# Kernel tuning notes

Hardware: AMD Instinct MI355X
Metric: run time of the kernel (lower is better)

The kernel has to match this reference:

```python
import jax, jax.numpy as jnp
import numpy as np

N_NODES = 100000
N_EDGES = 1600000
N_GRAPHS = 512
NEG_SLOPE = 0.2  # PyG GATConv default


def setup_inputs() -> dict:
    key = jax.random.key(0)
    ks = jax.random.split(key, 12)
    x = jax.random.normal(ks[0], (N_NODES, 75), dtype=jnp.float32)
    edge_index = jax.random.randint(ks[1], (2, N_EDGES), 0, N_NODES, dtype=jnp.int64 if jax.config.jax_enable_x64 else jnp.int32)
    batch = jnp.sort(jax.random.randint(ks[2], (N_NODES,), 0, N_GRAPHS, dtype=jnp.int32))
    s = lambda k, shp, fan: jax.random.normal(k, shp, dtype=jnp.float32) * (1.0 / np.sqrt(fan))
    return {
        "x": x, "edge_index": edge_index, "batch": batch,
        "W1": s(ks[3], (75, 64), 75),           # conv1: heads=8, out=8
        "att_src1": s(ks[4], (8, 8), 8),
        "att_dst1": s(ks[5], (8, 8), 8),
        "bias1": jnp.zeros((64,), jnp.float32),
        "W2": s(ks[6], (64, 128), 64),          # conv2: heads=1, out=128
        "att_src2": s(ks[7], (1, 128), 128),
        "att_dst2": s(ks[8], (1, 128), 128),
        "bias2": jnp.zeros((128,), jnp.float32),
        "Wg": s(ks[9], (128, 1), 128),
        "bg": jnp.zeros((1,), jnp.float32),
    }


def _gat_conv(x, src, dst, W, att_src, att_dst, bias, heads, out_ch):
    # x: [N, F_in]; edges src->dst (self-loops already included)
    n = x.shape[0]
    h = (x @ W).reshape(n, heads, out_ch)            # [N, H, C]
    a_src = (h * att_src).sum(-1)                    # [N, H]
    a_dst = (h * att_dst).sum(-1)                    # [N, H]
    e = a_src[src] + a_dst[dst]                      # [E, H]
    e = jax.nn.leaky_relu(e, NEG_SLOPE)
    # segment softmax over incoming edges of each dst node
    emax = jax.ops.segment_max(e, dst, num_segments=n)      # [N, H]
    ee = jnp.exp(e - emax[dst])
    denom = jax.ops.segment_sum(ee, dst, num_segments=n)    # [N, H]
    alpha = ee / denom[dst]                                  # [E, H]
    msg = h[src] * alpha[:, :, None]                          # [E, H, C]
    out = jax.ops.segment_sum(msg, dst, num_segments=n)      # [N, H, C]
    return out.reshape(n, heads * out_ch) + bias


def reference(x, edge_index, batch, W1, att_src1, att_dst1, bias1,
              W2, att_src2, att_dst2, bias2, Wg, bg):
    n = x.shape[0]
    # PyG GATConv adds self-loops by default
    loops = jnp.arange(n, dtype=edge_index.dtype)
    src = jnp.concatenate([edge_index[0], loops])
    dst = jnp.concatenate([edge_index[1], loops])
    # eval mode: dropout is identity
    x2 = jax.nn.elu(_gat_conv(x, src, dst, W1, att_src1, att_dst1, bias1, heads=8, out_ch=8))
    x4 = _gat_conv(x2, src, dst, W2, att_src2, att_dst2, bias2, heads=1, out_ch=128)
    y = jax.ops.segment_sum(x4, batch, num_segments=N_GRAPHS)  # global_add_pool
    return y @ Wg + bg  # [N_GRAPHS, 1]
```

## Files before the change

### kernel.cpp

```cpp
#include <hip/hip_runtime.h>
#include <hip/hip_bf16.h>
#include <math.h>

#define N_NODES 100000
#define N_EDGES 1600000
#define ET (N_EDGES + N_NODES)
#define N_GRAPHS 512
#define NEG_SLOPE 0.2f
#define G1_BLOCKS 2048
#define G2_BLOCKS 1280
#define F1_BLOCKS 2048

#define BSH 8
#define NBUCK ((N_NODES + 255) / 256)
#define BCAP 5120
#define ABLK 1024
#define CHUNK ((ET + ABLK - 1) / ABLK)

__device__ __forceinline__ void atomAddF(float* p, float v) { unsafeAtomicAdd(p, v); }
__device__ __forceinline__ float lrelu(float v) { return v >= 0.f ? v : NEG_SLOPE * v; }

__device__ __forceinline__ unsigned short f2bf(float f) {
    unsigned int u = __float_as_uint(f);
    u += 0x7FFFu + ((u >> 16) & 1u);
    return (unsigned short)(u >> 16);
}
__device__ __forceinline__ float bf2f(unsigned short s) { return __uint_as_float(((unsigned int)s) << 16); }
__device__ __forceinline__ float bflo(unsigned int p) { return __uint_as_float(p << 16); }
__device__ __forceinline__ float bfhi(unsigned int p) { return __uint_as_float(p & 0xFFFF0000u); }

__global__ __launch_bounds__(256) void k_pre(
    const int* __restrict__ ei, uint2* __restrict__ gbuf, int* __restrict__ bcur,
    const float* __restrict__ W2, const float* __restrict__ as2,
    const float* __restrict__ ad2, const float* __restrict__ Wg,
    const float* __restrict__ b2, const float* __restrict__ bg,
    float* __restrict__ wv, float* __restrict__ out)
{
    __shared__ __align__(16) char smem[CHUNK * 8 + NBUCK * 16];
    const int t = threadIdx.x;

    if (blockIdx.x >= ABLK) {
        const int bb = blockIdx.x - ABLK;
        if (bb > 0) {
            int i = (bb - 1) * 256 + t;
            if (i < N_GRAPHS) out[i] = bg[0];
            return;
        }
        if (t < 192) {
            int c = t & 63, which = t >> 6;
            const float* v = (which == 0) ? Wg : ((which == 1) ? as2 : ad2);
            float s = 0.f;
            #pragma unroll
            for (int k = 0; k < 128; ++k) s += W2[c * 128 + k] * v[k];
            wv[which * 64 + c] = s;
        } else if (t == 192) {
            float s = 0.f;
            #pragma unroll
            for (int k = 0; k < 128; ++k) s += b2[k] * Wg[k];
            wv[192] = s;
        }
        return;
    }

    uint2* pairs = (uint2*)smem;
    int* hist  = (int*)(smem + CHUNK * 8);
    int* excl  = hist + NBUCK;
    int* gbase = excl + NBUCK;
    int* cnt2  = gbase + NBUCK;
    const long e0 = (long)blockIdx.x * CHUNK;
    const int  n  = (int)((e0 + CHUNK <= ET) ? CHUNK : (ET - e0));
    for (int i = t; i < NBUCK; i += 256) { hist[i] = 0; cnt2[i] = 0; }
    __syncthreads();
    for (int i = t; i < n; i += 256) {
        long e = e0 + i;
        int dst = (e < N_EDGES) ? ei[N_EDGES + e] : (int)(e - N_EDGES);
        atomicAdd(&hist[dst >> BSH], 1);
    }
    __syncthreads();
    if (t == 0) {
        int acc = 0;
        for (int b = 0; b < NBUCK; ++b) { excl[b] = acc; acc += hist[b]; }
    }
    __syncthreads();
    for (int i = t; i < n; i += 256) {
        long e = e0 + i;
        int src, dst;
        if (e < N_EDGES) { src = ei[e]; dst = ei[N_EDGES + e]; }
        else             { src = dst = (int)(e - N_EDGES); }
        int b = dst >> BSH;
        int pos = excl[b] + atomicAdd(&cnt2[b], 1);
        pairs[pos] = make_uint2((unsigned)src, (unsigned)dst);
    }
    __syncthreads();
    for (int b = t; b < NBUCK; b += 256)
        gbase[b] = hist[b] ? atomicAdd(&bcur[b], hist[b]) : 0;
    __syncthreads();
    for (int i = t; i < n; i += 256) {
        uint2 pr = pairs[i];
        int b = (int)(pr.y >> BSH);
        gbuf[(long)b * BCAP + gbase[b] + (i - excl[b])] = pr;
    }
}

__global__ __launch_bounds__(256) void k_mid(
    const uint2* __restrict__ gbuf, const int* __restrict__ bcur,
    int* __restrict__ rowptr, int* __restrict__ ecol,
    const float* __restrict__ x, const float* __restrict__ W1,
    const float* __restrict__ as1, const float* __restrict__ ad1,
    unsigned short* __restrict__ h1p, unsigned short* __restrict__ a1sh,
    float* __restrict__ a1d)
{
    __shared__ __align__(16) char smem[4096];
    const int t = threadIdx.x;

    if (blockIdx.x >= NBUCK) {
        float (*xs)[76] = (float (*)[76])smem;
        const int g = t >> 6;
        const int c = t & 63;
        const int vb = blockIdx.x - NBUCK;
        for (int nb = vb; nb < N_NODES / 4; nb += F1_BLOCKS) {
            const int n = nb * 4 + g;
            const float* xr = x + (long)n * 75;
            xs[g][c] = xr[c];
            if (c < 11) xs[g][64 + c] = xr[64 + c];
            __syncthreads();
            float h = 0.f;
            #pragma unroll
            for (int k = 0; k < 75; ++k) h += xs[g][k] * W1[k * 64 + c];
            h1p[(long)n * 64 + c] = f2bf(h);
            const int head = c >> 3, lane = c & 7;
            float vs = h * as1[c];
            float vd = h * ad1[c];
            #pragma unroll
            for (int off = 1; off < 8; off <<= 1) {
                vs += __shfl_xor(vs, off, 64);
                vd += __shfl_xor(vd, off, 64);
            }
            if (lane == 0) { a1sh[n * 8 + head] = f2bf(vs); a1d[n * 8 + head] = vd; }
            __syncthreads();
        }
        return;
    }

    int* hist = (int*)smem;
    int* excl = hist + 256;
    int* cnt2 = excl + 256;
    int* red  = cnt2 + 256;
    const int b = blockIdx.x;
    const int cnt  = bcur[b];
    const int d0 = b << BSH;
    const int nloc = (N_NODES - d0 < 256) ? (N_NODES - d0) : 256;

    int partial = 0;
    for (int i = t; i < b; i += 256) partial += bcur[i];
    red[t] = partial;
    __syncthreads();
    for (int off = 128; off > 0; off >>= 1) {
        if (t < off) red[t] += red[t + off];
        __syncthreads();
    }
    const int base = red[0];

    if (t < nloc) { hist[t] = 0; cnt2[t] = 0; }
    __syncthreads();
    const uint2* eb = gbuf + (long)b * BCAP;
    for (int i = t; i < cnt; i += 256) atomicAdd(&hist[(int)eb[i].y - d0], 1);
    __syncthreads();
    if (t == 0) {
        int acc = 0;
        for (int k = 0; k < nloc; ++k) { excl[k] = acc; acc += hist[k]; }
    }
    __syncthreads();
    if (t < nloc) rowptr[d0 + t] = base + excl[t];
    if (b == NBUCK - 1 && t == 0) rowptr[N_NODES] = base + cnt;
    for (int i = t; i < cnt; i += 256) {
        uint2 pr = eb[i];
        int dl = (int)pr.y - d0;
        int slot = excl[dl] + atomicAdd(&cnt2[dl], 1);
        ecol[base + slot] = (int)pr.x;
    }
}

__global__ __launch_bounds__(256) void k_gat1(
    const int* __restrict__ rowptr, const int* __restrict__ ecol,
    const unsigned short* __restrict__ a1sh, const float* __restrict__ a1d,
    const unsigned short* __restrict__ h1p, const float* __restrict__ bias1,
    const float* __restrict__ wv,
    float2* __restrict__ sg2, float* __restrict__ a2dv)
{
    const int slot = threadIdx.x >> 6;
    const int lane = threadIdx.x & 63;
    const int g = lane >> 3;
    const int l = lane & 7;
    const int stride = gridDim.x * 4;

    for (int base = blockIdx.x * 4; base < N_NODES; base += stride) {
        const int dst = base + slot;
        const int beg = rowptr[dst], end = rowptr[dst + 1];
        const float adh = a1d[(long)dst * 8 + l];

        float acc[8] = {0.f,0.f,0.f,0.f,0.f,0.f,0.f,0.f};
        float den = 0.f;

        int j = beg + g;
        bool v = (j < end);
        int s = v ? ecol[j] : 0;
        unsigned short ab = a1sh[(long)s * 8 + l];
        uint4 pv = *(const uint4*)(h1p + (long)s * 64 + l * 8);

        for (int j0 = beg; j0 < end; j0 += 8) {
            int jn = j + 8;
            bool vn = (jn < end);
            int sn = vn ? ecol[jn] : 0;
            unsigned short abn = a1sh[(long)sn * 8 + l];
            uint4 pvn = *(const uint4*)(h1p + (long)sn * 64 + l * 8);
            float ee = v ? __expf(lrelu(bf2f(ab) + adh)) : 0.f;
            den += ee;
            acc[0] += ee * bflo(pv.x); acc[1] += ee * bfhi(pv.x);
            acc[2] += ee * bflo(pv.y); acc[3] += ee * bfhi(pv.y);
            acc[4] += ee * bflo(pv.z); acc[5] += ee * bfhi(pv.z);
            acc[6] += ee * bflo(pv.w); acc[7] += ee * bfhi(pv.w);
            j = jn; v = vn; s = sn; ab = abn; pv = pvn;
        }
        #pragma unroll
        for (int off = 8; off <= 32; off <<= 1) {
            den += __shfl_xor(den, off, 64);
            #pragma unroll
            for (int k = 0; k < 8; ++k) acc[k] += __shfl_xor(acc[k], off, 64);
        }

        if (g == 0) {
            const float inv = 1.f / den;
            float pg = 0.f, ps = 0.f, pd = 0.f;
            #pragma unroll
            for (int k = 0; k < 8; ++k) {
                float vv = acc[k] * inv + bias1[l * 8 + k];
                vv = vv > 0.f ? vv : (__expf(vv) - 1.f);
                pg += vv * wv[l * 8 + k];
                ps += vv * wv[64 + l * 8 + k];
                pd += vv * wv[128 + l * 8 + k];
            }
            #pragma unroll
            for (int off = 1; off < 8; off <<= 1) {
                pg += __shfl_xor(pg, off, 64);
                ps += __shfl_xor(ps, off, 64);
                pd += __shfl_xor(pd, off, 64);
            }
            if (l == 0) { sg2[dst] = make_float2(ps, pg); a2dv[dst] = pd; }
        }
    }
}

__global__ __launch_bounds__(256) void k_gat2(
    const int* __restrict__ rowptr, const int* __restrict__ ecol,
    const float2* __restrict__ sg2, const float* __restrict__ a2dv,
    const float* __restrict__ wv, const int* __restrict__ batch,
    float* __restrict__ out)
{
    const int lane = threadIdx.x & 63;
    const int sl = lane & 15;
    const int sgid = ((blockIdx.x * 256 + threadIdx.x) >> 4);
    const int NS = G2_BLOCKS * 16;
    const int per = (N_NODES + NS - 1) / NS;
    const int n0 = sgid * per;
    const int n1 = min(n0 + per, N_NODES);
    const float bc = wv[192];

    float accg = 0.f;
    int curg = -1;
    for (int n = n0; n < n1; ++n) {
        const int beg = rowptr[n], end = rowptr[n + 1];
        const float adv = a2dv[n];
        float num = 0.f, den = 0.f;
        for (int j = beg + sl; j < end; j += 16) {
            int s = ecol[j];
            float2 v = sg2[s];
            float ee = __expf(lrelu(v.x + adv));
            den += ee;
            num += ee * v.y;
        }
        #pragma unroll
        for (int off = 1; off < 16; off <<= 1) {
            den += __shfl_xor(den, off, 64);
            num += __shfl_xor(num, off, 64);
        }
        if (sl == 0) {
            int gr = batch[n];
            if (gr != curg) {
                if (curg >= 0) atomAddF(out + curg, accg);
                curg = gr; accg = 0.f;
            }
            accg += num / den + bc;
        }
    }
    if (sl == 0 && curg >= 0) atomAddF(out + curg, accg);
}

extern "C" void kernel_launch(void* const* d_in, const int* in_sizes, int n_in,
                              void* d_out, int out_size, void* d_ws, size_t ws_size,
                              hipStream_t stream) {
    (void)in_sizes; (void)n_in; (void)out_size; (void)ws_size;
    const float* x     = (const float*)d_in[0];
    const int*   ei    = (const int*)d_in[1];
    const int*   batch = (const int*)d_in[2];
    const float* W1    = (const float*)d_in[3];
    const float* as1   = (const float*)d_in[4];
    const float* ad1   = (const float*)d_in[5];
    const float* b1    = (const float*)d_in[6];
    const float* W2    = (const float*)d_in[7];
    const float* as2   = (const float*)d_in[8];
    const float* ad2   = (const float*)d_in[9];
    const float* b2    = (const float*)d_in[10];
    const float* Wg    = (const float*)d_in[11];
    const float* bg    = (const float*)d_in[12];
    float* out = (float*)d_out;

    const long N = N_NODES;
    char* p = (char*)d_ws;
    int* rowptr = (int*)p;              p += (N + 4)        * sizeof(int);
    int* bcur   = (int*)p;              p += 512            * sizeof(int);
    int* ecol   = (int*)p;              p += (long)ET       * sizeof(int);
    uint2* gbuf = (uint2*)p;            p += (long)NBUCK * BCAP * sizeof(uint2);
    unsigned short* h1p  = (unsigned short*)p; p += N * 64  * sizeof(unsigned short);
    unsigned short* a1sh = (unsigned short*)p; p += N * 8   * sizeof(unsigned short);
    float* a1d  = (float*)p;            p += N * 8          * sizeof(float);
    float2* sg2 = (float2*)p;           p += N              * sizeof(float2);
    float* a2dv = (float*)p;            p += N              * sizeof(float);
    float* wv   = (float*)p;            p += 256            * sizeof(float);

    hipMemsetAsync(bcur, 0, NBUCK * sizeof(int), stream);
    k_pre <<<ABLK + 3, 256, 0, stream>>>(ei, gbuf, bcur,
                                         W2, as2, ad2, Wg, b2, bg, wv, out);
    k_mid <<<NBUCK + F1_BLOCKS, 256, 0, stream>>>(gbuf, bcur, rowptr, ecol,
                                                  x, W1, as1, ad1, h1p, a1sh, a1d);
    k_gat1<<<G1_BLOCKS, 256, 0, stream>>>(rowptr, ecol, a1sh, a1d, h1p, b1, wv, sg2, a2dv);
    k_gat2<<<G2_BLOCKS, 256, 0, stream>>>(rowptr, ecol, sg2, a2dv, wv, batch, out);
}
```

Before: 311.8 us.

## Fuse CSR bucket finalize into gat1 and move x@W1 into pre kernel

Moves the first-layer feature transform into the edge-bucketing kernel, so it runs alongside the histogram work. It also fuses the per-bucket CSR build into the first GAT kernel, keeping each bucket's column list in LDS for the aggregation. Buckets shrink to 128 destinations and the single-thread serial prefix scans become parallel scans. This removes one launch and the global ecol re-read in gat1, but leaves only one block per 128 nodes, with 512 threads and larger LDS use, which may limit occupancy and load balance.

After: 281.2 us. 1.11x faster.

```diff
diff --git a/kernel.cpp b/kernel.cpp
--- a/kernel.cpp
+++ b/kernel.cpp
@@ -7,15 +7,16 @@
 #define ET (N_EDGES + N_NODES)
 #define N_GRAPHS 512
 #define NEG_SLOPE 0.2f
-#define G1_BLOCKS 2048
 #define G2_BLOCKS 1280
-#define F1_BLOCKS 2048
-
-#define BSH 8
-#define NBUCK ((N_NODES + 255) / 256)
-#define BCAP 5120
-#define ABLK 1024
+
+#define BSH 7
+#define NDB 128
+#define NBUCK ((N_NODES + NDB - 1) / NDB)
+#define BCAP 2560
+#define ABLK 512
 #define CHUNK ((ET + ABLK - 1) / ABLK)
+#define F1_OFF (ABLK + 3)
+#define PRE_GRID (F1_OFF + 1536)
 
 __device__ __forceinline__ void atomAddF(float* p, float v) { unsafeAtomicAdd(p, v); }
 __device__ __forceinline__ float lrelu(float v) { return v >= 0.f ? v : NEG_SLOPE * v; }
@@ -31,33 +32,67 @@
 
 __global__ __launch_bounds__(256) void k_pre(
     const int* __restrict__ ei, uint2* __restrict__ gbuf, int* __restrict__ bcur,
+    const float* __restrict__ x, const float* __restrict__ W1,
+    const float* __restrict__ as1, const float* __restrict__ ad1,
     const float* __restrict__ W2, const float* __restrict__ as2,
     const float* __restrict__ ad2, const float* __restrict__ Wg,
     const float* __restrict__ b2, const float* __restrict__ bg,
-    float* __restrict__ wv, float* __restrict__ out)
+    unsigned short* __restrict__ h1p, unsigned short* __restrict__ a1sh,
+    float* __restrict__ a1d, float* __restrict__ wv, float* __restrict__ out)
 {
-    __shared__ __align__(16) char smem[CHUNK * 8 + NBUCK * 16];
+    __shared__ __align__(16) char smem[CHUNK * 8 + NBUCK * 16 + 1024];
     const int t = threadIdx.x;
-
-    if (blockIdx.x >= ABLK) {
-        const int bb = blockIdx.x - ABLK;
-        if (bb > 0) {
+    const int blk = blockIdx.x;
+
+    if (blk >= ABLK && blk < F1_OFF) {
+        const int bb = blk - ABLK;
+        if (bb == 0) {
+            if (t < 192) {
+                int c = t & 63, which = t >> 6;
+                const float* v = (which == 0) ? Wg : ((which == 1) ? as2 : ad2);
+                float s = 0.f;
+                #pragma unroll
+                for (int k = 0; k < 128; ++k) s += W2[c * 128 + k] * v[k];
+                wv[which * 64 + c] = s;
+            } else if (t == 192) {
+                float s = 0.f;
+                #pragma unroll
+                for (int k = 0; k < 128; ++k) s += b2[k] * Wg[k];
+                wv[192] = s;
+            }
+        } else {
             int i = (bb - 1) * 256 + t;
             if (i < N_GRAPHS) out[i] = bg[0];
-            return;
-        }
-        if (t < 192) {
-            int c = t & 63, which = t >> 6;
-            const float* v = (which == 0) ? Wg : ((which == 1) ? as2 : ad2);
-            float s = 0.f;
-            #pragma unroll
-            for (int k = 0; k < 128; ++k) s += W2[c * 128 + k] * v[k];
-            wv[which * 64 + c] = s;
-        } else if (t == 192) {
-            float s = 0.f;
-            #pragma unroll
-            for (int k = 0; k < 128; ++k) s += b2[k] * Wg[k];
-            wv[192] = s;
+        }
+        return;
+    }
+
+    if (blk >= F1_OFF) {
+        float (*xs)[76] = (float (*)[76])smem;
+        const int g = t >> 6;
+        const int c = t & 63;
+        const int vb = blk - F1_OFF;
+        const int fstride = PRE_GRID - F1_OFF;
+        for (int nb = vb; nb < N_NODES / 4; nb += fstride) {
+            const int n = nb * 4 + g;
+            const float* xr = x + (long)n * 75;
+            xs[g][c] = xr[c];
+            if (c < 11) xs[g][64 + c] = xr[64 + c];
+            __syncthreads();
+            float h = 0.f;
+            #pragma unroll
+            for (int k = 0; k < 75; ++k) h += xs[g][k] * W1[k * 64 + c];
+            h1p[(long)n * 64 + c] = f2bf(h);
+            const int head = c >> 3, lane = c & 7;
+            float vs = h * as1[c];
+            float vd = h * ad1[c];
+            #pragma unroll
+            for (int off = 1; off < 8; off <<= 1) {
+                vs += __shfl_xor(vs, off, 64);
+                vd += __shfl_xor(vd, off, 64);
+            }
+            if (lane == 0) { a1sh[n * 8 + head] = f2bf(vs); a1d[n * 8 + head] = vd; }
+            __syncthreads();
         }
         return;
     }
@@ -67,7 +102,8 @@
     int* excl  = hist + NBUCK;
     int* gbase = excl + NBUCK;
     int* cnt2  = gbase + NBUCK;
-    const long e0 = (long)blockIdx.x * CHUNK;
+    int* red   = cnt2 + NBUCK;
+    const long e0 = (long)blk * CHUNK;
     const int  n  = (int)((e0 + CHUNK <= ET) ? CHUNK : (ET - e0));
     for (int i = t; i < NBUCK; i += 256) { hist[i] = 0; cnt2[i] = 0; }
     __syncthreads();
@@ -77,9 +113,28 @@
         atomicAdd(&hist[dst >> BSH], 1);
     }
     __syncthreads();
-    if (t == 0) {
-        int acc = 0;
-        for (int b = 0; b < NBUCK; ++b) { excl[b] = acc; acc += hist[b]; }
+    {
+        int lk[4]; int s = 0;
+        #pragma unroll
+        for (int k = 0; k < 4; ++k) {
+            int idx = t * 4 + k;
+            int v = (idx < NBUCK) ? hist[idx] : 0;
+            lk[k] = s; s += v;
+        }
+        red[t] = s;
+        __syncthreads();
+        for (int off = 1; off < 256; off <<= 1) {
+            int a = (t >= off) ? red[t - off] : 0;
+            __syncthreads();
+            red[t] += a;
+            __syncthreads();
+        }
+        int p = red[t] - s;
+        #pragma unroll
+        for (int k = 0; k < 4; ++k) {
+            int idx = t * 4 + k;
+            if (idx < NBUCK) excl[idx] = p + lk[k];
+        }
     }
     __syncthreads();
     for (int i = t; i < n; i += 256) {
@@ -102,101 +157,71 @@
     }
 }
 
-__global__ __launch_bounds__(256) void k_mid(
+__global__ __launch_bounds__(512) void k_gat1(
     const uint2* __restrict__ gbuf, const int* __restrict__ bcur,
     int* __restrict__ rowptr, int* __restrict__ ecol,
-    const float* __restrict__ x, const float* __restrict__ W1,
-    const float* __restrict__ as1, const float* __restrict__ ad1,
-    unsigned short* __restrict__ h1p, unsigned short* __restrict__ a1sh,
-    float* __restrict__ a1d)
-{
-    __shared__ __align__(16) char smem[4096];
-    const int t = threadIdx.x;
-
-    if (blockIdx.x >= NBUCK) {
-        float (*xs)[76] = (float (*)[76])smem;
-        const int g = t >> 6;
-        const int c = t & 63;
-        const int vb = blockIdx.x - NBUCK;
-        for (int nb = vb; nb < N_NODES / 4; nb += F1_BLOCKS) {
-            const int n = nb * 4 + g;
-            const float* xr = x + (long)n * 75;
-            xs[g][c] = xr[c];
-            if (c < 11) xs[g][64 + c] = xr[64 + c];
-            __syncthreads();
-            float h = 0.f;
-            #pragma unroll
-            for (int k = 0; k < 75; ++k) h += xs[g][k] * W1[k * 64 + c];
-            h1p[(long)n * 64 + c] = f2bf(h);
-            const int head = c >> 3, lane = c & 7;
-            float vs = h * as1[c];
-            float vd = h * ad1[c];
-            #pragma unroll
-            for (int off = 1; off < 8; off <<= 1) {
-                vs += __shfl_xor(vs, off, 64);
-                vd += __shfl_xor(vd, off, 64);
-            }
-            if (lane == 0) { a1sh[n * 8 + head] = f2bf(vs); a1d[n * 8 + head] = vd; }
-            __syncthreads();
-        }
-        return;
-    }
-
-    int* hist = (int*)smem;
-    int* excl = hist + 256;
-    int* cnt2 = excl + 256;
-    int* red  = cnt2 + 256;
-    const int b = blockIdx.x;
-    const int cnt  = bcur[b];
-    const int d0 = b << BSH;
-    const int nloc = (N_NODES - d0 < 256) ? (N_NODES - d0) : 256;
-
-    int partial = 0;
-    for (int i = t; i < b; i += 256) partial += bcur[i];
-    red[t] = partial;
-    __syncthreads();
-    for (int off = 128; off > 0; off >>= 1) {
-        if (t < off) red[t] += red[t + off];
-        __syncthreads();
-    }
-    const int base = red[0];
-
-    if (t < nloc) { hist[t] = 0; cnt2[t] = 0; }
-    __syncthreads();
-    const uint2* eb = gbuf + (long)b * BCAP;
-    for (int i = t; i < cnt; i += 256) atomicAdd(&hist[(int)eb[i].y - d0], 1);
-    __syncthreads();
-    if (t == 0) {
-        int acc = 0;
-        for (int k = 0; k < nloc; ++k) { excl[k] = acc; acc += hist[k]; }
-    }
-    __syncthreads();
-    if (t < nloc) rowptr[d0 + t] = base + excl[t];
-    if (b == NBUCK - 1 && t == 0) rowptr[N_NODES] = base + cnt;
-    for (int i = t; i < cnt; i += 256) {
-        uint2 pr = eb[i];
-        int dl = (int)pr.y - d0;
-        int slot = excl[dl] + atomicAdd(&cnt2[dl], 1);
-        ecol[base + slot] = (int)pr.x;
-    }
-}
-
-__global__ __launch_bounds__(256) void k_gat1(
-    const int* __restrict__ rowptr, const int* __restrict__ ecol,
     const unsigned short* __restrict__ a1sh, const float* __restrict__ a1d,
     const unsigned short* __restrict__ h1p, const float* __restrict__ bias1,
     const float* __restrict__ wv,
     float2* __restrict__ sg2, float* __restrict__ a2dv)
 {
-    const int slot = threadIdx.x >> 6;
-    const int lane = threadIdx.x & 63;
+    __shared__ int lds_ecol[BCAP];
+    __shared__ int hist[NDB], excl[NDB + 1], cnt2[NDB];
+    __shared__ int red[512];
+    const int t = threadIdx.x;
+    const int b = blockIdx.x;
+    const int d0 = b << BSH;
+    const int nloc = (N_NODES - d0 < NDB) ? (N_NODES - d0) : NDB;
+    const int cnt = bcur[b];
+
+    int partial = 0;
+    for (int i = t; i < b; i += 512) partial += bcur[i];
+    red[t] = partial;
+    __syncthreads();
+    for (int off = 256; off > 0; off >>= 1) {
+        if (t < off) red[t] += red[t + off];
+        __syncthreads();
+    }
+    const int base = red[0];
+    __syncthreads();
+
+    if (t < NDB) { hist[t] = 0; cnt2[t] = 0; }
+    __syncthreads();
+    const uint2* eb = gbuf + (long)b * BCAP;
+    for (int i = t; i < cnt; i += 512) atomicAdd(&hist[(int)eb[i].y - d0], 1);
+    __syncthreads();
+    {
+        int v = (t < NDB) ? hist[t] : 0;
+        if (t < NDB) red[t] = v;
+        __syncthreads();
+        for (int off = 1; off < NDB; off <<= 1) {
+            int a = (t < NDB && t >= off) ? red[t - off] : 0;
+            __syncthreads();
+            if (t < NDB) red[t] += a;
+            __syncthreads();
+        }
+        if (t < nloc) excl[t] = red[t] - v;
+        if (t == 0) excl[nloc] = cnt;
+    }
+    __syncthreads();
+    if (t < nloc) rowptr[d0 + t] = base + excl[t];
+    if (b == NBUCK - 1 && t == 0) rowptr[N_NODES] = base + cnt;
+    for (int i = t; i < cnt; i += 512) {
+        uint2 pr = eb[i];
+        int dl = (int)pr.y - d0;
+        int slot = excl[dl] + atomicAdd(&cnt2[dl], 1);
+        lds_ecol[slot] = (int)pr.x;
+    }
+    __syncthreads();
+    for (int i = t; i < cnt; i += 512) ecol[base + i] = lds_ecol[i];
+
+    const int wave = t >> 6;
+    const int lane = t & 63;
     const int g = lane >> 3;
     const int l = lane & 7;
-    const int stride = gridDim.x * 4;
-
-    for (int base = blockIdx.x * 4; base < N_NODES; base += stride) {
-        const int dst = base + slot;
-        const int beg = rowptr[dst], end = rowptr[dst + 1];
+    for (int di = wave; di < nloc; di += 8) {
+        const int dst = d0 + di;
+        const int beg = excl[di], end = excl[di + 1];
         const float adh = a1d[(long)dst * 8 + l];
 
         float acc[8] = {0.f,0.f,0.f,0.f,0.f,0.f,0.f,0.f};
@@ -204,14 +229,14 @@
 
         int j = beg + g;
         bool v = (j < end);
-        int s = v ? ecol[j] : 0;
+        int s = v ? lds_ecol[j] : 0;
         unsigned short ab = a1sh[(long)s * 8 + l];
         uint4 pv = *(const uint4*)(h1p + (long)s * 64 + l * 8);
 
         for (int j0 = beg; j0 < end; j0 += 8) {
             int jn = j + 8;
             bool vn = (jn < end);
-            int sn = vn ? ecol[jn] : 0;
+            int sn = vn ? lds_ecol[jn] : 0;
             unsigned short abn = a1sh[(long)sn * 8 + l];
             uint4 pvn = *(const uint4*)(h1p + (long)sn * 64 + l * 8);
             float ee = v ? __expf(lrelu(bf2f(ab) + adh)) : 0.f;
@@ -318,7 +343,7 @@
     const long N = N_NODES;
     char* p = (char*)d_ws;
     int* rowptr = (int*)p;              p += (N + 4)        * sizeof(int);
-    int* bcur   = (int*)p;              p += 512            * sizeof(int);
+    int* bcur   = (int*)p;              p += 1024           * sizeof(int);
     int* ecol   = (int*)p;              p += (long)ET       * sizeof(int);
     uint2* gbuf = (uint2*)p;            p += (long)NBUCK * BCAP * sizeof(uint2);
     unsigned short* h1p  = (unsigned short*)p; p += N * 64  * sizeof(unsigned short);
@@ -329,10 +354,10 @@
     float* wv   = (float*)p;            p += 256            * sizeof(float);
 
     hipMemsetAsync(bcur, 0, NBUCK * sizeof(int), stream);
-    k_pre <<<ABLK + 3, 256, 0, stream>>>(ei, gbuf, bcur,
-                                         W2, as2, ad2, Wg, b2, bg, wv, out);
-    k_mid <<<NBUCK + F1_BLOCKS, 256, 0, stream>>>(gbuf, bcur, rowptr, ecol,
-                                                  x, W1, as1, ad1, h1p, a1sh, a1d);
-    k_gat1<<<G1_BLOCKS, 256, 0, stream>>>(rowptr, ecol, a1sh, a1d, h1p, b1, wv, sg2, a2dv);
+    k_pre <<<PRE_GRID, 256, 0, stream>>>(ei, gbuf, bcur, x, W1, as1, ad1,
+                                         W2, as2, ad2, Wg, b2, bg,
+                                         h1p, a1sh, a1d, wv, out);
+    k_gat1<<<NBUCK, 512, 0, stream>>>(gbuf, bcur, rowptr, ecol,
+                                      a1sh, a1d, h1p, b1, wv, sg2, a2dv);
     k_gat2<<<G2_BLOCKS, 256, 0, stream>>>(rowptr, ecol, sg2, a2dv, wv, batch, out);
 }
```
